# Kernel optimization log

Measured on AMD Instinct MI355X. Metric: run time of the kernel, lower is better.

Reference implementation:

```python
import jax, jax.numpy as jnp
import numpy as np

B = 8192
H = 1024            # hidden_size
A = 512             # alphabet_size
S = 2               # sequence_length
D_IN = A * S        # 1024, gate input dim
D1, D2 = H // 2, H // 3   # decoder dims: 512, 341
TEMP = 1.0


def _linear_params(key, out_d, in_d):
    kw, kb = jax.random.split(key)
    lim = 1.0 / np.sqrt(in_d)
    W = jax.random.uniform(kw, (out_d, in_d), minval=-lim, maxval=lim, dtype=jnp.float32)
    b = jax.random.uniform(kb, (out_d,), minval=-lim, maxval=lim, dtype=jnp.float32)
    return W, b


def setup_inputs() -> dict:
    key = jax.random.key(0)
    ks = jax.random.split(key, 16)
    inp = {
        'x': jax.random.normal(ks[0], (B, D_IN), dtype=jnp.float32),
        'h': jax.random.normal(ks[1], (B, H), dtype=jnp.float32),
        'c': jax.random.normal(ks[2], (B, H), dtype=jnp.float32),
    }
    names = [('W_fi', 'b_fi', H, D_IN), ('W_fh', 'b_fh', H, H),
             ('W_ii', 'b_ii', H, D_IN), ('W_ih', 'b_ih', H, H),
             ('W_si', 'b_si', H, D_IN), ('W_sh', 'b_sh', H, H),
             ('W_oi', 'b_oi', H, D_IN), ('W_oh', 'b_oh', H, H),
             ('W_d1', 'b_d1', D1, H), ('W_d2', 'b_d2', D2, D1),
             ('W_d3', 'b_d3', A, D2)]
    for k, (wn, bn, od, idm) in zip(ks[3:3 + len(names)], names):
        W, b = _linear_params(k, od, idm)
        inp[wn] = W
        inp[bn] = b
    return inp


def reference(x, h, c,
              W_fi, b_fi, W_fh, b_fh,
              W_ii, b_ii, W_ih, b_ih,
              W_si, b_si, W_sh, b_sh,
              W_oi, b_oi, W_oh, b_oh,
              W_d1, b_d1, W_d2, b_d2, W_d3, b_d3):
    def lin(v, W, b):
        return v @ W.T + b

    f = jax.nn.sigmoid(lin(x, W_fi, b_fi) + lin(h, W_fh, b_fh))
    i = jax.nn.sigmoid(lin(x, W_ii, b_ii) + lin(h, W_ih, b_ih))
    s = jnp.tanh(lin(x, W_si, b_si) + lin(h, W_sh, b_sh))
    o = jax.nn.sigmoid(lin(x, W_oi, b_oi) + lin(h, W_oh, b_oh))
    c_new = c * f + i * s
    h_new = o * jnp.tanh(c_new)
    d = jnp.tanh(lin(h_new, W_d1, b_d1))
    d = jnp.tanh(lin(d, W_d2, b_d2))
    d = jax.nn.softmax(lin(d, W_d3, b_d3) / TEMP, axis=-1)
    return h_new, d
```

## Files before the change

### kernel.cpp

```cpp
#include <hip/hip_runtime.h>
#include <cstdint>
#include <cstddef>


typedef _Float16 half_t;
typedef _Float16 half8 __attribute__((ext_vector_type(8)));
typedef _Float16 half4v __attribute__((ext_vector_type(4)));
typedef float float4v __attribute__((ext_vector_type(4)));

#define GLD_LDS16(gptr, lptr)                                                  \
  __builtin_amdgcn_global_load_lds(                                            \
      (const __attribute__((address_space(1))) void*)(gptr),                   \
      (__attribute__((address_space(3))) void*)(lptr), 16, 0, 0)

__device__ __forceinline__ float fsig(float x) {
  return 1.0f / (1.0f + __expf(-x));
}
__device__ __forceinline__ float ftanh_(float x) {
  const float e = __expf(2.0f * x);
  return 1.0f - 2.0f / (e + 1.0f);
}

__global__ __launch_bounds__(512, 2) void gemm_gates(const half_t* __restrict__ A,
                                                     const half_t* __restrict__ Bw,
                                                     const float* __restrict__ bias,
                                                     const float* __restrict__ cin,
                                                     float* __restrict__ hout,
                                                     half_t* __restrict__ h2f) {
  constexpr int K = 2048;
  constexpr int NT = 64;
  __shared__ alignas(16) half_t As[3][256 * 32];
  __shared__ alignas(16) half_t Bs[3][256 * 32];
  const int tid = threadIdx.x;
  const int lane = tid & 63;
  const int wave = tid >> 6;
  const int m = lane & 15;
  const int q = lane >> 4;
  const int ks = (q ^ ((m >> 1) & 3)) << 3;
  const int wm = (wave >> 2) << 7;
  const int wn = (wave & 3) << 6;

  const int bid = blockIdx.x;
  const int xcd = bid & 7;
  const int l = bid >> 3;
  const size_t tile_n = (size_t)((xcd << 1) | (l & 1)) << 8;
  const size_t tile_m = (size_t)(l >> 1) << 8;

  const int ci0 = tid, ci1 = tid + 512;
  const int r0 = ci0 >> 2, k0s = (ci0 & 3) ^ ((r0 >> 1) & 3);
  const int r1 = ci1 >> 2, k1s = (ci1 & 3) ^ ((r1 >> 1) & 3);
  const half_t* Ag0 = A + (tile_m + r0) * (size_t)K + k0s * 8;
  const half_t* Ag1 = A + (tile_m + r1) * (size_t)K + k1s * 8;
  const half_t* Bg0 = Bw + (tile_n + r0) * (size_t)K + k0s * 8;
  const half_t* Bg1 = Bw + (tile_n + r1) * (size_t)K + k1s * 8;
  const int p0 = ci0 * 16, p1 = ci1 * 16;

  GLD_LDS16(Ag0, (char*)As[0] + p0);
  GLD_LDS16(Ag1, (char*)As[0] + p1);
  GLD_LDS16(Bg0, (char*)Bs[0] + p0);
  GLD_LDS16(Bg1, (char*)Bs[0] + p1);
  GLD_LDS16(Ag0 + 32, (char*)As[1] + p0);
  GLD_LDS16(Ag1 + 32, (char*)As[1] + p1);
  GLD_LDS16(Bg0 + 32, (char*)Bs[1] + p0);
  GLD_LDS16(Bg1 + 32, (char*)Bs[1] + p1);
  asm volatile("s_waitcnt vmcnt(4)" ::: "memory");
  __builtin_amdgcn_s_barrier();
  __builtin_amdgcn_sched_barrier(0);

  float4v acc[8][4] = {};
  int bc = 0;
  for (int t = 0; t < NT; ++t) {
    const half_t* as = As[bc];
    const half_t* bs = Bs[bc];
    const int bst = (bc + 2 >= 3) ? bc - 1 : bc + 2;
    const size_t koff = (size_t)(t + 2) * 32;
    half8 af[4], bf[4];
#pragma unroll
    for (int i = 0; i < 4; ++i)
      af[i] = *(const half8*)(as + (wm + i * 16 + m) * 32 + ks);
#pragma unroll
    for (int j = 0; j < 4; ++j)
      bf[j] = *(const half8*)(bs + (wn + j * 16 + m) * 32 + ks);
    if (t < NT - 2) {
      GLD_LDS16(Ag0 + koff, (char*)As[bst] + p0);
      GLD_LDS16(Ag1 + koff, (char*)As[bst] + p1);
    }
    __builtin_amdgcn_s_barrier();
    asm volatile("s_waitcnt lgkmcnt(0)" ::: "memory");
    __builtin_amdgcn_sched_barrier(0);
    __builtin_amdgcn_s_setprio(1);
#pragma unroll
    for (int i = 0; i < 4; ++i)
#pragma unroll
      for (int j = 0; j < 4; ++j)
        acc[i][j] = __builtin_amdgcn_mfma_f32_16x16x32_f16(af[i], bf[j],
                                                           acc[i][j], 0, 0, 0);
    __builtin_amdgcn_s_setprio(0);
    __builtin_amdgcn_s_barrier();
    __builtin_amdgcn_sched_barrier(0);
    half8 ag[4];
#pragma unroll
    for (int i = 0; i < 4; ++i)
      ag[i] = *(const half8*)(as + (wm + 64 + i * 16 + m) * 32 + ks);
    if (t < NT - 2) {
      GLD_LDS16(Bg0 + koff, (char*)Bs[bst] + p0);
      GLD_LDS16(Bg1 + koff, (char*)Bs[bst] + p1);
    }
    __builtin_amdgcn_s_barrier();
    asm volatile("s_waitcnt lgkmcnt(0)" ::: "memory");
    __builtin_amdgcn_sched_barrier(0);
    __builtin_amdgcn_s_setprio(1);
#pragma unroll
    for (int i = 0; i < 4; ++i)
#pragma unroll
      for (int j = 0; j < 4; ++j)
        acc[4 + i][j] = __builtin_amdgcn_mfma_f32_16x16x32_f16(
            ag[i], bf[j], acc[4 + i][j], 0, 0, 0);
    __builtin_amdgcn_s_setprio(0);
    if (t < NT - 2) {
      asm volatile("s_waitcnt vmcnt(4)" ::: "memory");
    } else if (t == NT - 2) {
      asm volatile("s_waitcnt vmcnt(0)" ::: "memory");
    }
    __builtin_amdgcn_s_barrier();
    __builtin_amdgcn_sched_barrier(0);
    bc = (bc + 1 == 3) ? 0 : bc + 1;
  }

  const int nwave = (int)tile_n + wn;
  const int u = ((nwave >> 6) << 4) + m;
  const int rtb = (int)((tile_m + wm) >> 4);
  const int ubase = (u >> 5) * 512 + ((u >> 3) & 3) * 128 + (u & 7);
  float bg[4];
#pragma unroll
  for (int g = 0; g < 4; ++g) bg[g] = bias[nwave + g * 16 + m];
#pragma unroll
  for (int i = 0; i < 8; ++i) {
#pragma unroll
    for (int r = 0; r < 4; ++r) {
      const size_t row = tile_m + wm + q * 4 + i * 16 + r;
      const size_t off = row * 1024 + u;
      const float F = fsig(acc[i][0][r] + bg[0]);
      const float I = fsig(acc[i][1][r] + bg[1]);
      const float S = ftanh_(acc[i][2][r] + bg[2]);
      const float O = fsig(acc[i][3][r] + bg[3]);
      const float cn = cin[off] * F + I * S;
      const float hn = O * ftanh_(cn);
      hout[off] = hn;
      h2f[(size_t)(rtb + i) * 16384 + ubase + (q * 4 + r) * 8] = (half_t)hn;
    }
  }
}

template <int K, int OUTK, int MODE>
__global__ __launch_bounds__(256) void dec_layer(const half_t* __restrict__ Af,
                                                 const half_t* __restrict__ W,
                                                 const float* __restrict__ bias,
                                                 void* __restrict__ outp) {
  constexpr int KP = K + 8;
  constexpr int CH = K / 8;
  constexpr int ITER = 32 * CH / 256;
  __shared__ alignas(16) half_t Wl[32 * KP];
  const int tid = threadIdx.x;
  const int lane = tid & 63;
  const int w = tid >> 6;
  const int m = lane & 15;
  const int q = lane >> 4;
  const int g = blockIdx.x;

#pragma unroll
  for (int it = 0; it < ITER; ++it) {
    const int ci = it * 256 + tid;
    const int c = ci / CH;
    const int kq = ci - c * CH;
    const half8 v = *(const half8*)(W + ((size_t)(g * 32 + c)) * K + kq * 8);
    *(half8*)(Wl + c * KP + kq * 8) = v;
  }
  __syncthreads();

  const int rt0 = blockIdx.y * 8 + w * 2;
  const half_t* a0 = Af + (size_t)rt0 * (16 * K) + lane * 8;
  const half_t* a1 = a0 + 16 * K;
  float4v acc[2][2] = {};
#pragma unroll 2
  for (int kk = 0; kk < K; kk += 32) {
    const half8 af0 = *(const half8*)(a0 + kk * 16);
    const half8 af1 = *(const half8*)(a1 + kk * 16);
    half8 bf[2];
#pragma unroll
    for (int j = 0; j < 2; ++j)
      bf[j] = *(const half8*)(Wl + (j * 16 + m) * KP + kk + q * 8);
    acc[0][0] = __builtin_amdgcn_mfma_f32_16x16x32_f16(af0, bf[0], acc[0][0], 0, 0, 0);
    acc[0][1] = __builtin_amdgcn_mfma_f32_16x16x32_f16(af0, bf[1], acc[0][1], 0, 0, 0);
    acc[1][0] = __builtin_amdgcn_mfma_f32_16x16x32_f16(af1, bf[0], acc[1][0], 0, 0, 0);
    acc[1][1] = __builtin_amdgcn_mfma_f32_16x16x32_f16(af1, bf[1], acc[1][1], 0, 0, 0);
  }

#pragma unroll
  for (int t = 0; t < 2; ++t) {
    const int rt = rt0 + t;
#pragma unroll
    for (int j = 0; j < 2; ++j) {
      const int col = g * 32 + j * 16 + m;
      const float bv = bias[col];
      if (MODE == 0) {
        half_t* of = (half_t*)outp;
        const size_t base = (size_t)rt * (16 * OUTK) + g * 512 +
                            (j * 2 + (m >> 3)) * 128 + (m & 7);
#pragma unroll
        for (int r = 0; r < 4; ++r)
          of[base + (q * 4 + r) * 8] = (half_t)ftanh_(acc[t][j][r] + bv);
      } else {
        float* ol = (float*)outp;
#pragma unroll
        for (int r = 0; r < 4; ++r)
          ol[((size_t)rt * 16 + q * 4 + r) * 512 + col] = acc[t][j][r] + bv;
      }
    }
  }
}

__global__ __launch_bounds__(256) void softmax512(const float* __restrict__ logits,
                                                  float* __restrict__ out) {
  const int row = blockIdx.x * 4 + (threadIdx.x >> 6);
  const int lane = threadIdx.x & 63;
  const float4v* src = (const float4v*)(logits + (size_t)row * 512);
  const float4v v0 = src[lane * 2];
  const float4v v1 = src[lane * 2 + 1];
  float mx = fmaxf(fmaxf(fmaxf(v0.x, v0.y), fmaxf(v0.z, v0.w)),
                   fmaxf(fmaxf(v1.x, v1.y), fmaxf(v1.z, v1.w)));
#pragma unroll
  for (int off = 32; off > 0; off >>= 1) mx = fmaxf(mx, __shfl_xor(mx, off, 64));
  const float e0 = __expf(v0.x - mx), e1 = __expf(v0.y - mx);
  const float e2 = __expf(v0.z - mx), e3 = __expf(v0.w - mx);
  const float e4 = __expf(v1.x - mx), e5 = __expf(v1.y - mx);
  const float e6 = __expf(v1.z - mx), e7 = __expf(v1.w - mx);
  float sum = ((e0 + e1) + (e2 + e3)) + ((e4 + e5) + (e6 + e7));
#pragma unroll
  for (int off = 32; off > 0; off >>= 1) sum += __shfl_xor(sum, off, 64);
  const float inv = 1.0f / sum;
  float4v o0, o1;
  o0.x = e0 * inv; o0.y = e1 * inv; o0.z = e2 * inv; o0.w = e3 * inv;
  o1.x = e4 * inv; o1.y = e5 * inv; o1.z = e6 * inv; o1.w = e7 * inv;
  float4v* dst = (float4v*)(out + (size_t)row * 512);
  dst[lane * 2] = o0;
  dst[lane * 2 + 1] = o1;
}

__global__ void prep_pack(const float* __restrict__ x, const float* __restrict__ h,
                          const float* __restrict__ Wfi, const float* __restrict__ Wfh,
                          const float* __restrict__ Wii, const float* __restrict__ Wih,
                          const float* __restrict__ Wsi, const float* __restrict__ Wsh,
                          const float* __restrict__ Woi, const float* __restrict__ Woh,
                          half_t* __restrict__ xh, half_t* __restrict__ wall) {
  const int bid = blockIdx.x;
  const float* src;
  half_t* dst;
  size_t idx;
  if (bid < 16384) {
    idx = ((size_t)bid * 256 + threadIdx.x) * 4;
    const size_t b = idx >> 11;
    const int col = (int)(idx & 2047);
    src = (col < 1024) ? (x + b * 1024 + col) : (h + b * 1024 + (col - 1024));
    dst = xh + idx;
  } else {
    idx = ((size_t)(bid - 16384) * 256 + threadIdx.x) * 4;
    const int n = (int)(idx >> 11);
    const int col = (int)(idx & 2047);
    const int g = (n >> 4) & 3;
    const size_t u = (size_t)(((n >> 6) << 4) | (n & 15));
    const float* Wi = (g == 0) ? Wfi : (g == 1) ? Wii : (g == 2) ? Wsi : Woi;
    const float* Wh = (g == 0) ? Wfh : (g == 1) ? Wih : (g == 2) ? Wsh : Woh;
    src = (col < 1024) ? (Wi + u * 1024 + col) : (Wh + u * 1024 + (col - 1024));
    dst = wall + idx;
  }
  const float4v v = *(const float4v*)src;
  half4v o;
  o.x = (half_t)v.x; o.y = (half_t)v.y; o.z = (half_t)v.z; o.w = (half_t)v.w;
  *(half4v*)dst = o;
}

__global__ void prep_small(const float* __restrict__ Wd1, const float* __restrict__ Wd2,
                           const float* __restrict__ Wd3, const float* __restrict__ bd2,
                           const float* __restrict__ bfi, const float* __restrict__ bfh,
                           const float* __restrict__ bii, const float* __restrict__ bih,
                           const float* __restrict__ bsi, const float* __restrict__ bsh,
                           const float* __restrict__ boi, const float* __restrict__ boh,
                           half_t* __restrict__ WD1, half_t* __restrict__ WD2h,
                           half_t* __restrict__ WD3h, float* __restrict__ BALL,
                           float* __restrict__ BD2) {
  const int bid = blockIdx.x;
  const int tid = threadIdx.x;
  if (bid < 512) {
    const size_t i4 = ((size_t)bid * 256 + tid) * 4;
    const float4v v = *(const float4v*)(Wd1 + i4);
    half4v o;
    o.x = (half_t)v.x; o.y = (half_t)v.y; o.z = (half_t)v.z; o.w = (half_t)v.w;
    *(half4v*)(WD1 + i4) = o;
  } else if (bid < 704) {
    const size_t i4 = ((size_t)(bid - 512) * 256 + tid) * 4;
    const int r = (int)(i4 >> 9);
    const int cc = (int)(i4 & 511);
    half4v o;
    if (r < 341) {
      const float4v v = *(const float4v*)(Wd2 + (size_t)r * 512 + cc);
      o.x = (half_t)v.x; o.y = (half_t)v.y; o.z = (half_t)v.z; o.w = (half_t)v.w;
    } else {
      o.x = (half_t)0.f; o.y = (half_t)0.f; o.z = (half_t)0.f; o.w = (half_t)0.f;
    }
    *(half4v*)(WD2h + i4) = o;
  } else if (bid < 896) {
    const size_t i4 = ((size_t)(bid - 704) * 256 + tid) * 4;
    const int r = (int)(i4 / 384);
    const int cc = (int)(i4 - (size_t)r * 384);
    half4v o;
    o.x = (cc + 0 < 341) ? (half_t)Wd3[(size_t)r * 341 + cc + 0] : (half_t)0.f;
    o.y = (cc + 1 < 341) ? (half_t)Wd3[(size_t)r * 341 + cc + 1] : (half_t)0.f;
    o.z = (cc + 2 < 341) ? (half_t)Wd3[(size_t)r * 341 + cc + 2] : (half_t)0.f;
    o.w = (cc + 3 < 341) ? (half_t)Wd3[(size_t)r * 341 + cc + 3] : (half_t)0.f;
    *(half4v*)(WD3h + i4) = o;
  } else if (bid < 912) {
    const int n = (bid - 896) * 256 + tid;
    const int g = (n >> 4) & 3;
    const int u = ((n >> 6) << 4) | (n & 15);
    const float* bi = (g == 0) ? bfi : (g == 1) ? bii : (g == 2) ? bsi : boi;
    const float* bh = (g == 0) ? bfh : (g == 1) ? bih : (g == 2) ? bsh : boh;
    BALL[n] = bi[u] + bh[u];
  } else {
    const int i = (bid - 912) * 256 + tid;
    if (i < 384) BD2[i] = (i < 341) ? bd2[i] : 0.0f;
  }
}

extern "C" void kernel_launch(void* const* d_in, const int* in_sizes, int n_in,
                              void* d_out, int out_size, void* d_ws, size_t ws_size,
                              hipStream_t stream) {
  const float* x = (const float*)d_in[0];
  const float* h = (const float*)d_in[1];
  const float* c = (const float*)d_in[2];
  const float* Wfi = (const float*)d_in[3];  const float* bfi = (const float*)d_in[4];
  const float* Wfh = (const float*)d_in[5];  const float* bfh = (const float*)d_in[6];
  const float* Wii = (const float*)d_in[7];  const float* bii = (const float*)d_in[8];
  const float* Wih = (const float*)d_in[9];  const float* bih = (const float*)d_in[10];
  const float* Wsi = (const float*)d_in[11]; const float* bsi = (const float*)d_in[12];
  const float* Wsh = (const float*)d_in[13]; const float* bsh = (const float*)d_in[14];
  const float* Woi = (const float*)d_in[15]; const float* boi = (const float*)d_in[16];
  const float* Woh = (const float*)d_in[17]; const float* boh = (const float*)d_in[18];
  const float* Wd1 = (const float*)d_in[19]; const float* bd1 = (const float*)d_in[20];
  const float* Wd2 = (const float*)d_in[21]; const float* bd2 = (const float*)d_in[22];
  const float* Wd3 = (const float*)d_in[23]; const float* bd3 = (const float*)d_in[24];

  char* ws = (char*)d_ws;
  size_t o = 0;
  auto alloc = [&](size_t bytes) {
    size_t cur = o;
    o += (bytes + 255) & ~(size_t)255;
    return cur;
  };
  half_t* XH   = (half_t*)(ws + alloc((size_t)8192 * 2048 * 2));
  half_t* WALL = (half_t*)(ws + alloc((size_t)4096 * 2048 * 2));
  float*  BALL = (float*)(ws + alloc(4096 * 4));
  half_t* WD1  = (half_t*)(ws + alloc((size_t)512 * 1024 * 2));
  half_t* WD2  = (half_t*)(ws + alloc((size_t)384 * 512 * 2));
  float*  BD2  = (float*)(ws + alloc(384 * 4));
  half_t* WD3  = (half_t*)(ws + alloc((size_t)512 * 384 * 2));
  half_t* H2F  = (half_t*)(ws + alloc((size_t)8192 * 1024 * 2));
  half_t* D1F  = (half_t*)(ws + alloc((size_t)8192 * 512 * 2));
  half_t* D2F  = (half_t*)(ws + alloc((size_t)8192 * 384 * 2));
  float*  LOG  = (float*)XH;

  float* h_out = (float*)d_out;
  float* d_outp = (float*)d_out + (size_t)8192 * 1024;

  prep_pack<<<24576, 256, 0, stream>>>(x, h, Wfi, Wfh, Wii, Wih, Wsi, Wsh, Woi, Woh,
                                       XH, WALL);
  prep_small<<<914, 256, 0, stream>>>(Wd1, Wd2, Wd3, bd2, bfi, bfh, bii, bih, bsi, bsh,
                                      boi, boh, WD1, WD2, WD3, BALL, BD2);

  gemm_gates<<<512, 512, 0, stream>>>(XH, WALL, BALL, c, h_out, H2F);

  dec_layer<1024, 512, 0><<<dim3(16, 64), 256, 0, stream>>>(H2F, WD1, bd1, D1F);
  dec_layer<512, 384, 0><<<dim3(12, 64), 256, 0, stream>>>(D1F, WD2, BD2, D2F);
  dec_layer<384, 512, 1><<<dim3(16, 64), 256, 0, stream>>>(D2F, WD3, bd3, LOG);
  softmax512<<<2048, 256, 0, stream>>>(LOG, d_outp);
}
```

Measured before the change: 403.9 us.

## Fuse three decoder layers and softmax into one kernel with LDS-resident activations

Replaces the three per-layer decoder GEMM kernels and the separate softmax kernel with a single kernel. Each block handles 32 rows, keeps the intermediate activations and logits in LDS, and writes only the final softmax output. Weights are repacked at prep time into an MFMA fragment-friendly layout and read directly from global/L2 instead of being staged in LDS. This removes the intermediate global round trips and three launches. In exchange it uses only 256 blocks with large LDS per block, which limits occupancy and parallelism, and every block re-reads all decoder weights.

```diff
diff --git a/kernel.cpp b/kernel.cpp
--- a/kernel.cpp
+++ b/kernel.cpp
@@ -152,99 +152,157 @@
   }
 }
 
-template <int K, int OUTK, int MODE>
-__global__ __launch_bounds__(256) void dec_layer(const half_t* __restrict__ Af,
-                                                 const half_t* __restrict__ W,
-                                                 const float* __restrict__ bias,
-                                                 void* __restrict__ outp) {
-  constexpr int KP = K + 8;
-  constexpr int CH = K / 8;
-  constexpr int ITER = 32 * CH / 256;
-  __shared__ alignas(16) half_t Wl[32 * KP];
+__global__ __launch_bounds__(512, 2) void fused_decoder(
+    const half_t* __restrict__ h2f,
+    const half_t* __restrict__ W1f,
+    const float* __restrict__ b1,
+    const half_t* __restrict__ W2f,
+    const float* __restrict__ b2,
+    const half_t* __restrict__ W3f,
+    const float* __restrict__ b3,
+    float* __restrict__ out) {
+  __shared__ alignas(16) half_t A1s[2 * 16384];
+  __shared__ alignas(16) half_t A2s[2 * 8192];
+  __shared__ alignas(16) half_t A3s[2 * 6144];
+  float* LOGL = (float*)A1s;
+
   const int tid = threadIdx.x;
   const int lane = tid & 63;
   const int w = tid >> 6;
   const int m = lane & 15;
   const int q = lane >> 4;
-  const int g = blockIdx.x;
-
-#pragma unroll
-  for (int it = 0; it < ITER; ++it) {
-    const int ci = it * 256 + tid;
-    const int c = ci / CH;
-    const int kq = ci - c * CH;
-    const half8 v = *(const half8*)(W + ((size_t)(g * 32 + c)) * K + kq * 8);
-    *(half8*)(Wl + c * KP + kq * 8) = v;
-  }
+  const int b = blockIdx.x;
+
+  const half_t* src = h2f + (size_t)b * 32768;
+#pragma unroll
+  for (int it = 0; it < 8; ++it)
+    GLD_LDS16(src + (it * 512 + tid) * 8, (char*)A1s + (it * 512 + tid) * 16);
+  asm volatile("s_waitcnt vmcnt(0)" ::: "memory");
   __syncthreads();
 
-  const int rt0 = blockIdx.y * 8 + w * 2;
-  const half_t* a0 = Af + (size_t)rt0 * (16 * K) + lane * 8;
-  const half_t* a1 = a0 + 16 * K;
-  float4v acc[2][2] = {};
+  {
+    float4v acc[2][4] = {};
+    const half_t* w1 = W1f + (size_t)(w * 4) * 16384 + lane * 8;
 #pragma unroll 2
-  for (int kk = 0; kk < K; kk += 32) {
-    const half8 af0 = *(const half8*)(a0 + kk * 16);
-    const half8 af1 = *(const half8*)(a1 + kk * 16);
-    half8 bf[2];
-#pragma unroll
-    for (int j = 0; j < 2; ++j)
-      bf[j] = *(const half8*)(Wl + (j * 16 + m) * KP + kk + q * 8);
-    acc[0][0] = __builtin_amdgcn_mfma_f32_16x16x32_f16(af0, bf[0], acc[0][0], 0, 0, 0);
-    acc[0][1] = __builtin_amdgcn_mfma_f32_16x16x32_f16(af0, bf[1], acc[0][1], 0, 0, 0);
-    acc[1][0] = __builtin_amdgcn_mfma_f32_16x16x32_f16(af1, bf[0], acc[1][0], 0, 0, 0);
-    acc[1][1] = __builtin_amdgcn_mfma_f32_16x16x32_f16(af1, bf[1], acc[1][1], 0, 0, 0);
-  }
-
-#pragma unroll
-  for (int t = 0; t < 2; ++t) {
-    const int rt = rt0 + t;
-#pragma unroll
-    for (int j = 0; j < 2; ++j) {
-      const int col = g * 32 + j * 16 + m;
-      const float bv = bias[col];
-      if (MODE == 0) {
-        half_t* of = (half_t*)outp;
-        const size_t base = (size_t)rt * (16 * OUTK) + g * 512 +
-                            (j * 2 + (m >> 3)) * 128 + (m & 7);
+    for (int c = 0; c < 32; ++c) {
+      half8 wf[4], af[2];
+#pragma unroll
+      for (int j = 0; j < 4; ++j)
+        wf[j] = *(const half8*)(w1 + j * 16384 + c * 512);
+#pragma unroll
+      for (int rt = 0; rt < 2; ++rt)
+        af[rt] = *(const half8*)(A1s + rt * 16384 + c * 512 + q * 128 + m * 8);
+#pragma unroll
+      for (int rt = 0; rt < 2; ++rt)
+#pragma unroll
+        for (int j = 0; j < 4; ++j)
+          acc[rt][j] = __builtin_amdgcn_mfma_f32_16x16x32_f16(af[rt], wf[j],
+                                                              acc[rt][j], 0, 0, 0);
+    }
+#pragma unroll
+    for (int j = 0; j < 4; ++j) {
+      const int col = w * 64 + j * 16 + m;
+      const float bv = b1[col];
+      const int cb = (col >> 5) * 512 + ((col >> 3) & 3) * 128 + (col & 7);
+#pragma unroll
+      for (int rt = 0; rt < 2; ++rt)
 #pragma unroll
         for (int r = 0; r < 4; ++r)
-          of[base + (q * 4 + r) * 8] = (half_t)ftanh_(acc[t][j][r] + bv);
-      } else {
-        float* ol = (float*)outp;
+          A2s[rt * 8192 + cb + (q * 4 + r) * 8] = (half_t)ftanh_(acc[rt][j][r] + bv);
+    }
+  }
+  __syncthreads();
+
+  {
+    float4v acc[2][3] = {};
+    const half_t* w2 = W2f + (size_t)(w * 3) * 8192 + lane * 8;
+#pragma unroll 2
+    for (int c = 0; c < 16; ++c) {
+      half8 wf[3], af[2];
+#pragma unroll
+      for (int j = 0; j < 3; ++j)
+        wf[j] = *(const half8*)(w2 + j * 8192 + c * 512);
+#pragma unroll
+      for (int rt = 0; rt < 2; ++rt)
+        af[rt] = *(const half8*)(A2s + rt * 8192 + c * 512 + q * 128 + m * 8);
+#pragma unroll
+      for (int rt = 0; rt < 2; ++rt)
+#pragma unroll
+        for (int j = 0; j < 3; ++j)
+          acc[rt][j] = __builtin_amdgcn_mfma_f32_16x16x32_f16(af[rt], wf[j],
+                                                              acc[rt][j], 0, 0, 0);
+    }
+#pragma unroll
+    for (int j = 0; j < 3; ++j) {
+      const int col = w * 48 + j * 16 + m;
+      const float bv = b2[col];
+      const int cb = (col >> 5) * 512 + ((col >> 3) & 3) * 128 + (col & 7);
+#pragma unroll
+      for (int rt = 0; rt < 2; ++rt)
 #pragma unroll
         for (int r = 0; r < 4; ++r)
-          ol[((size_t)rt * 16 + q * 4 + r) * 512 + col] = acc[t][j][r] + bv;
-      }
-    }
-  }
-}
-
-__global__ __launch_bounds__(256) void softmax512(const float* __restrict__ logits,
-                                                  float* __restrict__ out) {
-  const int row = blockIdx.x * 4 + (threadIdx.x >> 6);
-  const int lane = threadIdx.x & 63;
-  const float4v* src = (const float4v*)(logits + (size_t)row * 512);
-  const float4v v0 = src[lane * 2];
-  const float4v v1 = src[lane * 2 + 1];
-  float mx = fmaxf(fmaxf(fmaxf(v0.x, v0.y), fmaxf(v0.z, v0.w)),
-                   fmaxf(fmaxf(v1.x, v1.y), fmaxf(v1.z, v1.w)));
-#pragma unroll
-  for (int off = 32; off > 0; off >>= 1) mx = fmaxf(mx, __shfl_xor(mx, off, 64));
-  const float e0 = __expf(v0.x - mx), e1 = __expf(v0.y - mx);
-  const float e2 = __expf(v0.z - mx), e3 = __expf(v0.w - mx);
-  const float e4 = __expf(v1.x - mx), e5 = __expf(v1.y - mx);
-  const float e6 = __expf(v1.z - mx), e7 = __expf(v1.w - mx);
-  float sum = ((e0 + e1) + (e2 + e3)) + ((e4 + e5) + (e6 + e7));
-#pragma unroll
-  for (int off = 32; off > 0; off >>= 1) sum += __shfl_xor(sum, off, 64);
-  const float inv = 1.0f / sum;
-  float4v o0, o1;
-  o0.x = e0 * inv; o0.y = e1 * inv; o0.z = e2 * inv; o0.w = e3 * inv;
-  o1.x = e4 * inv; o1.y = e5 * inv; o1.z = e6 * inv; o1.w = e7 * inv;
-  float4v* dst = (float4v*)(out + (size_t)row * 512);
-  dst[lane * 2] = o0;
-  dst[lane * 2 + 1] = o1;
+          A3s[rt * 6144 + cb + (q * 4 + r) * 8] = (half_t)ftanh_(acc[rt][j][r] + bv);
+    }
+  }
+  __syncthreads();
+
+  {
+    float4v acc[2][4] = {};
+    const half_t* w3 = W3f + (size_t)(w * 4) * 6144 + lane * 8;
+#pragma unroll 2
+    for (int c = 0; c < 12; ++c) {
+      half8 wf[4], af[2];
+#pragma unroll
+      for (int j = 0; j < 4; ++j)
+        wf[j] = *(const half8*)(w3 + j * 6144 + c * 512);
+#pragma unroll
+      for (int rt = 0; rt < 2; ++rt)
+        af[rt] = *(const half8*)(A3s + rt * 6144 + c * 512 + q * 128 + m * 8);
+#pragma unroll
+      for (int rt = 0; rt < 2; ++rt)
+#pragma unroll
+        for (int j = 0; j < 4; ++j)
+          acc[rt][j] = __builtin_amdgcn_mfma_f32_16x16x32_f16(af[rt], wf[j],
+                                                              acc[rt][j], 0, 0, 0);
+    }
+#pragma unroll
+    for (int j = 0; j < 4; ++j) {
+      const int col = w * 64 + j * 16 + m;
+      const float bv = b3[col];
+#pragma unroll
+      for (int rt = 0; rt < 2; ++rt)
+#pragma unroll
+        for (int r = 0; r < 4; ++r)
+          LOGL[(rt * 16 + q * 4 + r) * 512 + col] = acc[rt][j][r] + bv;
+    }
+  }
+  __syncthreads();
+
+#pragma unroll
+  for (int rr = 0; rr < 4; ++rr) {
+    const int row = w * 4 + rr;
+    const float4v* srcv = (const float4v*)(LOGL + row * 512);
+    const float4v v0 = srcv[lane * 2];
+    const float4v v1 = srcv[lane * 2 + 1];
+    float mx = fmaxf(fmaxf(fmaxf(v0.x, v0.y), fmaxf(v0.z, v0.w)),
+                     fmaxf(fmaxf(v1.x, v1.y), fmaxf(v1.z, v1.w)));
+#pragma unroll
+    for (int off = 32; off > 0; off >>= 1) mx = fmaxf(mx, __shfl_xor(mx, off, 64));
+    const float e0 = __expf(v0.x - mx), e1 = __expf(v0.y - mx);
+    const float e2 = __expf(v0.z - mx), e3 = __expf(v0.w - mx);
+    const float e4 = __expf(v1.x - mx), e5 = __expf(v1.y - mx);
+    const float e6 = __expf(v1.z - mx), e7 = __expf(v1.w - mx);
+    float sum = ((e0 + e1) + (e2 + e3)) + ((e4 + e5) + (e6 + e7));
+#pragma unroll
+    for (int off = 32; off > 0; off >>= 1) sum += __shfl_xor(sum, off, 64);
+    const float inv = 1.0f / sum;
+    float4v o0, o1;
+    o0.x = e0 * inv; o0.y = e1 * inv; o0.z = e2 * inv; o0.w = e3 * inv;
+    o1.x = e4 * inv; o1.y = e5 * inv; o1.z = e6 * inv; o1.w = e7 * inv;
+    float4v* dst = (float4v*)(out + ((size_t)b * 32 + row) * 512);
+    dst[lane * 2] = o0;
+    dst[lane * 2 + 1] = o1;
+  }
 }
 
 __global__ void prep_pack(const float* __restrict__ x, const float* __restrict__ h,
@@ -293,32 +351,40 @@
   const int tid = threadIdx.x;
   if (bid < 512) {
     const size_t i4 = ((size_t)bid * 256 + tid) * 4;
+    const int col = (int)(i4 >> 10);
+    const int k0 = (int)(i4 & 1023);
     const float4v v = *(const float4v*)(Wd1 + i4);
     half4v o;
     o.x = (half_t)v.x; o.y = (half_t)v.y; o.z = (half_t)v.z; o.w = (half_t)v.w;
-    *(half4v*)(WD1 + i4) = o;
+    const size_t fa = (size_t)(col >> 4) * 16384 + (k0 >> 5) * 512 +
+                      ((k0 >> 3) & 3) * 128 + (col & 15) * 8 + (k0 & 7);
+    *(half4v*)(WD1 + fa) = o;
   } else if (bid < 704) {
     const size_t i4 = ((size_t)(bid - 512) * 256 + tid) * 4;
-    const int r = (int)(i4 >> 9);
-    const int cc = (int)(i4 & 511);
+    const int col = (int)(i4 >> 9);
+    const int k0 = (int)(i4 & 511);
     half4v o;
-    if (r < 341) {
-      const float4v v = *(const float4v*)(Wd2 + (size_t)r * 512 + cc);
+    if (col < 341) {
+      const float4v v = *(const float4v*)(Wd2 + (size_t)col * 512 + k0);
       o.x = (half_t)v.x; o.y = (half_t)v.y; o.z = (half_t)v.z; o.w = (half_t)v.w;
     } else {
       o.x = (half_t)0.f; o.y = (half_t)0.f; o.z = (half_t)0.f; o.w = (half_t)0.f;
     }
-    *(half4v*)(WD2h + i4) = o;
+    const size_t fa = (size_t)(col >> 4) * 8192 + (k0 >> 5) * 512 +
+                      ((k0 >> 3) & 3) * 128 + (col & 15) * 8 + (k0 & 7);
+    *(half4v*)(WD2h + fa) = o;
   } else if (bid < 896) {
     const size_t i4 = ((size_t)(bid - 704) * 256 + tid) * 4;
-    const int r = (int)(i4 / 384);
-    const int cc = (int)(i4 - (size_t)r * 384);
+    const int col = (int)(i4 / 384);
+    const int k0 = (int)(i4 - (size_t)col * 384);
     half4v o;
-    o.x = (cc + 0 < 341) ? (half_t)Wd3[(size_t)r * 341 + cc + 0] : (half_t)0.f;
-    o.y = (cc + 1 < 341) ? (half_t)Wd3[(size_t)r * 341 + cc + 1] : (half_t)0.f;
-    o.z = (cc + 2 < 341) ? (half_t)Wd3[(size_t)r * 341 + cc + 2] : (half_t)0.f;
-    o.w = (cc + 3 < 341) ? (half_t)Wd3[(size_t)r * 341 + cc + 3] : (half_t)0.f;
-    *(half4v*)(WD3h + i4) = o;
+    o.x = (k0 + 0 < 341) ? (half_t)Wd3[(size_t)col * 341 + k0 + 0] : (half_t)0.f;
+    o.y = (k0 + 1 < 341) ? (half_t)Wd3[(size_t)col * 341 + k0 + 1] : (half_t)0.f;
+    o.z = (k0 + 2 < 341) ? (half_t)Wd3[(size_t)col * 341 + k0 + 2] : (half_t)0.f;
+    o.w = (k0 + 3 < 341) ? (half_t)Wd3[(size_t)col * 341 + k0 + 3] : (half_t)0.f;
+    const size_t fa = (size_t)(col >> 4) * 6144 + (k0 >> 5) * 512 +
+                      ((k0 >> 3) & 3) * 128 + (col & 15) * 8 + (k0 & 7);
+    *(half4v*)(WD3h + fa) = o;
   } else if (bid < 912) {
     const int n = (bid - 896) * 256 + tid;
     const int g = (n >> 4) & 3;
@@ -365,9 +431,6 @@
   float*  BD2  = (float*)(ws + alloc(384 * 4));
   half_t* WD3  = (half_t*)(ws + alloc((size_t)512 * 384 * 2));
   half_t* H2F  = (half_t*)(ws + alloc((size_t)8192 * 1024 * 2));
-  half_t* D1F  = (half_t*)(ws + alloc((size_t)8192 * 512 * 2));
-  half_t* D2F  = (half_t*)(ws + alloc((size_t)8192 * 384 * 2));
-  float*  LOG  = (float*)XH;
 
   float* h_out = (float*)d_out;
   float* d_outp = (float*)d_out + (size_t)8192 * 1024;
@@ -379,8 +442,5 @@
 
   gemm_gates<<<512, 512, 0, stream>>>(XH, WALL, BALL, c, h_out, H2F);
 
-  dec_layer<1024, 512, 0><<<dim3(16, 64), 256, 0, stream>>>(H2F, WD1, bd1, D1F);
-  dec_layer<512, 384, 0><<<dim3(12, 64), 256, 0, stream>>>(D1F, WD2, BD2, D2F);
-  dec_layer<384, 512, 1><<<dim3(16, 64), 256, 0, stream>>>(D2F, WD3, bd3, LOG);
-  softmax512<<<2048, 256, 0, stream>>>(LOG, d_outp);
-}
+  fused_decoder<<<256, 512, 0, stream>>>(H2F, WD1, bd1, WD2, BD2, WD3, bd3, d_outp);
+}
```

Result: faster. 384.3 us (-4.8%).
